# Kernel optimization log

Hardware: AMD Instinct MI355X
Metric: run time of the kernel (lower is better)

## Reference

```python
import jax, jax.numpy as jnp
import numpy as np

EPS = 1e-5
NUM_GROUPS = 16


def _deform_conv(x, offset, mask, weight):
    """Modulated deformable conv v2, 3x3, stride 1, pad 1, no bias.
    x: [B,C,H,W], offset: [B,18,H,W] (y,x interleaved per kernel point),
    mask: [B,9,H,W], weight: [O,C,3,3].
    """
    B, C, H, W = x.shape
    O = weight.shape[0]
    K = 9
    off = offset.reshape(B, K, 2, H, W)
    dy, dx = off[:, :, 0], off[:, :, 1]  # [B,K,H,W]
    # base sampling grid: output pixel + kernel tap offset (pad=1 -> taps -1..1)
    ky, kx = jnp.meshgrid(jnp.arange(3), jnp.arange(3), indexing='ij')
    ky = (ky.reshape(K) - 1).astype(x.dtype)
    kx = (kx.reshape(K) - 1).astype(x.dtype)
    iy = jnp.arange(H, dtype=x.dtype)[:, None]
    ix = jnp.arange(W, dtype=x.dtype)[None, :]
    py = iy[None, None] + ky[None, :, None, None] + dy  # [B,K,H,W]
    px = ix[None, None] + kx[None, :, None, None] + dx

    y0 = jnp.floor(py)
    x0 = jnp.floor(px)
    wy = py - y0  # grad flows to offsets via these weights
    wx = px - x0

    xf = x.reshape(B, C, H * W)

    def gather(yc, xc, w):
        # yc,xc,w: [B,K,H,W] float; returns weighted samples [B,C,K,H,W]
        valid = (yc >= 0) & (yc <= H - 1) & (xc >= 0) & (xc <= W - 1)
        yi = jnp.clip(yc, 0, H - 1).astype(jnp.int32)
        xi = jnp.clip(xc, 0, W - 1).astype(jnp.int32)
        idx = (yi * W + xi).reshape(B, K * H * W)
        g = jax.vmap(lambda xb, ib: xb[:, ib])(xf, idx)  # [B,C,K*H*W]
        g = g.reshape(B, C, K, H, W)
        wv = (w * valid.astype(x.dtype))[:, None]  # [B,1,K,H,W]
        return g * wv

    val = gather(y0, x0, (1 - wy) * (1 - wx))
    val = val + gather(y0, x0 + 1, (1 - wy) * wx)
    val = val + gather(y0 + 1, x0, wy * (1 - wx))
    val = val + gather(y0 + 1, x0 + 1, wy * wx)

    val = val * mask[:, None]  # modulation: [B,C,K,H,W] * [B,1,K,H,W]
    w = weight.reshape(O, C, K)
    return jnp.einsum('bckhw,ock->bohw', val, w)


def _group_norm(y, gamma, beta):
    B, O, H, W = y.shape
    g = y.reshape(B, NUM_GROUPS, O // NUM_GROUPS, H, W)
    mean = g.mean(axis=(2, 3, 4), keepdims=True)
    var = ((g - mean) ** 2).mean(axis=(2, 3, 4), keepdims=True)
    g = (g - mean) * jax.lax.rsqrt(var + EPS)
    y = g.reshape(B, O, H, W)
    return y * gamma[None, :, None, None] + beta[None, :, None, None]


def setup_inputs() -> dict:
    key = jax.random.key(0)
    k1, k2, k3, k4 = jax.random.split(key, 4)
    B, C, O, H, W = 8, 256, 256, 64, 64
    x = jax.random.normal(k1, (B, C, H, W), jnp.float32)
    offset = jax.random.normal(k2, (B, 18, H, W), jnp.float32)
    mask = jax.random.uniform(k3, (B, 9, H, W), jnp.float32)
    weight = jax.random.normal(k4, (O, C, 3, 3), jnp.float32) * 0.02
    gamma = jnp.ones((O,), jnp.float32)
    beta = jnp.zeros((O,), jnp.float32)
    return {"x": x, "offset": offset, "mask": mask, "weight": weight,
            "gamma": gamma, "beta": beta}


def reference(x, offset, mask, weight, gamma, beta):
    y = _deform_conv(x, offset, mask, weight)
    return _group_norm(y, gamma, beta)
```

## Files before the change

kernel.cpp:

```cpp
#include <hip/hip_runtime.h>
#include <hip/hip_fp16.h>
#include <math.h>

#define BB 8
#define CC 256
#define OO 256
#define HH 64
#define WW 64
#define KK 9
#define HWSZ 4096
#define CKSZ 2304
#define NG 16
#define OPG 16
#define EPSV 1e-5f

typedef _Float16 f16;
typedef f16 f16x8 __attribute__((ext_vector_type(8)));
typedef float f32x4 __attribute__((ext_vector_type(4)));

#define XH_ELEMS ((size_t)BB*HWSZ*CC)
#define WF_ELEMS ((size_t)OO*CKSZ)
#define CV_ELEMS ((size_t)BB*OO*HWSZ)
#define PSUM_FLOATS ((size_t)512*32)

__global__ __launch_bounds__(256) void x_transpose_k(
    const float* __restrict__ x, __half* __restrict__ xh)
{
  int blk = blockIdx.x;
  int b = blk >> 8; int rem = blk & 255;
  int c0 = (rem >> 6) * 64; int hw0 = (rem & 63) * 64;
  __shared__ float st[64][65];
  int t = threadIdx.x;
  #pragma unroll
  for (int i = 0; i < 16; ++i) {
    int idx = t + i*256; int c = idx >> 6, w = idx & 63;
    st[c][w] = x[((size_t)(b*CC + c0 + c))*HWSZ + hw0 + w];
  }
  __syncthreads();
  #pragma unroll
  for (int i = 0; i < 8; ++i) {
    int idx = t + i*256; int r = idx >> 5, cp = idx & 31;
    __half2 v = __floats2half2_rn(st[cp*2][r], st[cp*2+1][r]);
    *(__half2*)&xh[((size_t)(b*HWSZ) + hw0 + r)*CC + c0 + cp*2] = v;
  }
}

__global__ __launch_bounds__(256) void w_frag_k(
    const float* __restrict__ w, __half* __restrict__ wf)
{
  int i = blockIdx.x*256 + threadIdx.x;
  int e = i & 7, lane = (i >> 3) & 63, mi = (i >> 9) & 3;
  int ks = (i >> 11) & 1, wid = (i >> 12) & 3, cc = i >> 14;
  int k = cc >> 2, c0i = cc & 3;
  int o = wid*64 + mi*16 + (lane & 15);
  int c = c0i*64 + ks*32 + (lane >> 4)*8 + e;
  wf[i] = __float2half(w[(o*CC + c)*KK + k]);
}

template<int F16OUT>
__global__ __launch_bounds__(256, 3) void dcn_mfma_k(
    const float* __restrict__ off, const float* __restrict__ msk,
    const __half* __restrict__ xh, const __half* __restrict__ wf,
    float* __restrict__ out32, __half* __restrict__ conv16,
    float* __restrict__ psum)
{
  __shared__ __half sVl[2][64*64];
  __shared__ uint   sTapP[KK][64][4];
  __shared__ float  sRed[4][4][2];

  const int t = threadIdx.x;
  const int b = blockIdx.x & 7;
  const int h = blockIdx.x >> 3;

  const int lane = t & 63, wid = t >> 6;
  const int lr = lane & 15, lh = lane >> 4;
  const int gp = t >> 2, gq = t & 3;

  for (int s = t; s < KK*64; s += 256) {
    int k = s >> 6, p = s & 63;
    float dy = off[(((b*18) + 2*k    )*HH + h)*WW + p];
    float dx = off[(((b*18) + 2*k + 1)*HH + h)*WW + p];
    float m  = msk[(((b*KK) + k)*HH + h)*WW + p];
    float py = (float)(h + (k/3) - 1) + dy;
    float px = (float)(p + (k%3) - 1) + dx;
    float y0f = floorf(py), x0f = floorf(px);
    float wy = py - y0f, wx = px - x0f;
    int y0 = (int)y0f, x0 = (int)x0f;
    #pragma unroll
    for (int tap = 0; tap < 4; ++tap) {
      int yy = y0 + (tap >> 1), xx = x0 + (tap & 1);
      bool v = (yy >= 0) & (yy < HH) & (xx >= 0) & (xx < WW);
      float bw = ((tap >> 1) ? wy : 1.f - wy) * ((tap & 1) ? wx : 1.f - wx);
      float wgt = v ? bw * m : 0.f;
      int cy = min(max(yy, 0), HH-1), cx = min(max(xx, 0), WW-1);
      uint idx = (uint)(cy*WW + cx);
      sTapP[k][p][tap] = (idx << 16)
                       | (uint)__half_as_ushort(__float2half(wgt));
    }
  }
  __syncthreads();

  f32x4 acc[4][4];
  #pragma unroll
  for (int mi = 0; mi < 4; ++mi)
    #pragma unroll
    for (int ni = 0; ni < 4; ++ni) acc[mi][ni] = (f32x4){0.f,0.f,0.f,0.f};

  const char* xbase = (const char*)xh + (size_t)b * (HWSZ*CC*2);

  uint toff[4]; __half2 twv[4];
  #pragma unroll
  for (int i = 0; i < 4; ++i) {
    uint tp = sTapP[0][gp][i];
    toff[i] = (tp >> 16) << 9;
    twv[i]  = __half2half2(__ushort_as_half((unsigned short)(tp & 0xFFFFu)));
  }
  int tk = 0;

  auto combine_write = [&](uint4 r0, uint4 r1, uint4 r2, uint4 r3,
                           int oct, __half* dst) {
    const __half2* t0 = (const __half2*)&r0; const __half2* t1 = (const __half2*)&r1;
    const __half2* t2 = (const __half2*)&r2; const __half2* t3 = (const __half2*)&r3;
    __half2 o_[4];
    #pragma unroll
    for (int r = 0; r < 4; ++r)
      o_[r] = __hfma2(twv[0], t0[r], __hfma2(twv[1], t1[r],
              __hfma2(twv[2], t2[r], __hmul2(twv[3], t3[r]))));
    *(uint4*)&dst[gp*64 + ((oct ^ (gp & 7)) << 3)] = *(uint4*)o_;
  };

  {
    const char* cb = xbase + gq*16;
    uint4 a0 = *(const uint4*)(cb + toff[0]);
    uint4 a1 = *(const uint4*)(cb + toff[1]);
    uint4 a2 = *(const uint4*)(cb + toff[2]);
    uint4 a3 = *(const uint4*)(cb + toff[3]);
    uint4 b0 = *(const uint4*)(cb + toff[0] + 64);
    uint4 b1 = *(const uint4*)(cb + toff[1] + 64);
    uint4 b2 = *(const uint4*)(cb + toff[2] + 64);
    uint4 b3 = *(const uint4*)(cb + toff[3] + 64);
    combine_write(a0, a1, a2, a3, gq,     sVl[0]);
    combine_write(b0, b1, b2, b3, gq + 4, sVl[0]);
  }

  int cur = 0;
  for (int cc = 0; cc < 36; ++cc) {
    __syncthreads();

    const __half* wfp = wf + (size_t)(cc*4 + wid)*4096 + lane*8;
    f16x8 areg[2][4];
    #pragma unroll
    for (int ks = 0; ks < 2; ++ks)
      #pragma unroll
      for (int mi = 0; mi < 4; ++mi)
        areg[ks][mi] = *(const f16x8*)(wfp + (ks*4 + mi)*512);

    bool pf = (cc + 1 < 36);
    int kn = (cc+1) >> 2, c0n = ((cc+1) & 3) << 6;
    uint4 ga0, ga1, ga2, ga3, gb0, gb1, gb2, gb3;
    if (pf) {
      if (kn != tk) {
        #pragma unroll
        for (int i = 0; i < 4; ++i) {
          uint tp = sTapP[kn][gp][i];
          toff[i] = (tp >> 16) << 9;
          twv[i]  = __half2half2(__ushort_as_half((unsigned short)(tp & 0xFFFFu)));
        }
        tk = kn;
      }
      const char* cb = xbase + (size_t)(c0n*2) + gq*16;
      ga0 = *(const uint4*)(cb + toff[0]);
      ga1 = *(const uint4*)(cb + toff[1]);
      ga2 = *(const uint4*)(cb + toff[2]);
      ga3 = *(const uint4*)(cb + toff[3]);
      gb0 = *(const uint4*)(cb + toff[0] + 64);
      gb1 = *(const uint4*)(cb + toff[1] + 64);
      gb2 = *(const uint4*)(cb + toff[2] + 64);
      gb3 = *(const uint4*)(cb + toff[3] + 64);
    }

    #pragma unroll
    for (int ks = 0; ks < 2; ++ks) {
      f16x8 brg[4];
      #pragma unroll
      for (int ni = 0; ni < 4; ++ni) {
        int r = ni*16 + lr;
        brg[ni] = *(const f16x8*)&sVl[cur][r*64 + (((ks*4 + lh) ^ (r & 7)) << 3)];
      }
      #pragma unroll
      for (int mi = 0; mi < 4; ++mi)
        #pragma unroll
        for (int ni = 0; ni < 4; ++ni)
          acc[mi][ni] = __builtin_amdgcn_mfma_f32_16x16x32_f16(
              areg[ks][mi], brg[ni], acc[mi][ni], 0, 0, 0);
    }

    if (pf) {
      combine_write(ga0, ga1, ga2, ga3, gq,     sVl[cur ^ 1]);
      combine_write(gb0, gb1, gb2, gb3, gq + 4, sVl[cur ^ 1]);
      cur ^= 1;
    }
  }

  #pragma unroll
  for (int mi = 0; mi < 4; ++mi) {
    #pragma unroll
    for (int ni = 0; ni < 4; ++ni) {
      int ob = wid*64 + mi*16 + lh*4;
      int pp = ni*16 + lr;
      #pragma unroll
      for (int j = 0; j < 4; ++j) {
        size_t idx = ((size_t)(b*OO + ob + j))*HWSZ + h*WW + pp;
        if (F16OUT) conv16[idx] = __float2half(acc[mi][ni][j]);
        else        out32[idx] = acc[mi][ni][j];
      }
    }
  }

  if (F16OUT) {
    #pragma unroll
    for (int mi = 0; mi < 4; ++mi) {
      float s1 = 0.f, s2 = 0.f;
      #pragma unroll
      for (int ni = 0; ni < 4; ++ni)
        #pragma unroll
        for (int j = 0; j < 4; ++j) {
          float v = acc[mi][ni][j];
          s1 += v; s2 += v*v;
        }
      #pragma unroll
      for (int d = 32; d > 0; d >>= 1) {
        s1 += __shfl_xor(s1, d);
        s2 += __shfl_xor(s2, d);
      }
      if (lane == 0) { sRed[wid][mi][0] = s1; sRed[wid][mi][1] = s2; }
    }
    __syncthreads();
    if (t < 16) {
      psum[(size_t)blockIdx.x*32 + t*2]     = sRed[t >> 2][t & 3][0];
      psum[(size_t)blockIdx.x*32 + t*2 + 1] = sRed[t >> 2][t & 3][1];
    }
  }
}

__global__ __launch_bounds__(256) void gn_norm2_k(
    const __half* __restrict__ conv16, const float* __restrict__ psum,
    const float* __restrict__ gamma, const float* __restrict__ beta,
    float* __restrict__ out)
{
  int bid = blockIdx.x;
  int bo = bid >> 1;
  int b = bo >> 8, o = bo & 255;
  int g = o >> 4;
  float s1 = 0.f, s2 = 0.f;
  for (int hbl = 0; hbl < 64; ++hbl) {
    s1 += psum[(size_t)(hbl*8 + b)*32 + g*2];
    s2 += psum[(size_t)(hbl*8 + b)*32 + g*2 + 1];
  }
  const float invN = 1.f / (float)(OPG*HWSZ);
  float mean = s1 * invN;
  float var  = s2 * invN - mean*mean;
  float inv = rsqrtf(var + EPSV);
  float sc = gamma[o]*inv;
  float sh = beta[o] - mean*sc;

  size_t e0 = ((size_t)(b*OO + o))*HWSZ + (size_t)(bid & 1)*2048
            + (size_t)threadIdx.x*8;
  uint4 u = *(const uint4*)(conv16 + e0);
  const __half2* hh = (const __half2*)&u;
  float r[8];
  #pragma unroll
  for (int j = 0; j < 4; ++j) {
    float2 f = __half22float2(hh[j]);
    r[2*j] = f.x; r[2*j+1] = f.y;
  }
  *(float4*)&out[e0]     = make_float4(r[0]*sc+sh, r[1]*sc+sh, r[2]*sc+sh, r[3]*sc+sh);
  *(float4*)&out[e0 + 4] = make_float4(r[4]*sc+sh, r[5]*sc+sh, r[6]*sc+sh, r[7]*sc+sh);
}

__global__ __launch_bounds__(1024) void gn_stats_k(
    const float* __restrict__ out, float* __restrict__ stats)
{
  int bg = blockIdx.x;
  const float4* p = (const float4*)(out + (size_t)bg*OPG*HWSZ);
  const int n4 = OPG*HWSZ/4;
  float s1 = 0.f, s2 = 0.f;
  for (int i = threadIdx.x; i < n4; i += 1024) {
    float4 v = p[i];
    s1 += v.x + v.y + v.z + v.w;
    s2 += v.x*v.x + v.y*v.y + v.z*v.z + v.w*v.w;
  }
  #pragma unroll
  for (int o2 = 32; o2 > 0; o2 >>= 1) {
    s1 += __shfl_down(s1, o2);
    s2 += __shfl_down(s2, o2);
  }
  __shared__ float r1[16], r2[16];
  int wd = threadIdx.x >> 6, lane = threadIdx.x & 63;
  if (lane == 0) { r1[wd] = s1; r2[wd] = s2; }
  __syncthreads();
  if (threadIdx.x == 0) {
    float t1 = 0.f, t2 = 0.f;
    #pragma unroll
    for (int i = 0; i < 16; i++) { t1 += r1[i]; t2 += r2[i]; }
    const float invN = 1.f / (float)(OPG*HWSZ);
    float mean = t1 * invN;
    float var  = t2 * invN - mean*mean;
    stats[bg*2]   = mean;
    stats[bg*2+1] = var;
  }
}

__global__ __launch_bounds__(256) void gn_norm_k(
    float* __restrict__ out, const float* __restrict__ stats,
    const float* __restrict__ gamma, const float* __restrict__ beta)
{
  size_t i = (size_t)blockIdx.x*256 + threadIdx.x;
  const size_t n4 = (size_t)BB*OO*HWSZ/4;
  if (i >= n4) return;
  size_t base = i*4;
  int bo = (int)(base / HWSZ);
  int b = bo / OO, o = bo - b*OO;
  int g = o >> 4;
  float mean = stats[(b*NG+g)*2], var = stats[(b*NG+g)*2+1];
  float inv = rsqrtf(var + EPSV);
  float sc = gamma[o]*inv;
  float sh = beta[o] - mean*sc;
  float4 v = *(float4*)&out[base];
  v.x = v.x*sc + sh; v.y = v.y*sc + sh;
  v.z = v.z*sc + sh; v.w = v.w*sc + sh;
  *(float4*)&out[base] = v;
}

extern "C" void kernel_launch(void* const* d_in, const int* in_sizes, int n_in,
                              void* d_out, int out_size, void* d_ws, size_t ws_size,
                              hipStream_t stream) {
  const float* x      = (const float*)d_in[0];
  const float* offset = (const float*)d_in[1];
  const float* mask   = (const float*)d_in[2];
  const float* weight = (const float*)d_in[3];
  const float* gamma  = (const float*)d_in[4];
  const float* beta   = (const float*)d_in[5];
  float* out = (float*)d_out;

  __half* xh   = (__half*)d_ws;
  __half* wf   = xh + XH_ELEMS;
  __half* cv   = wf + WF_ELEMS;
  float* psum  = (float*)(cv + CV_ELEMS);

  const size_t need = (XH_ELEMS + WF_ELEMS + CV_ELEMS)*2 + PSUM_FLOATS*4 + 1024;

  x_transpose_k<<<BB*4*64, 256, 0, stream>>>(x, xh);
  w_frag_k<<<(int)(WF_ELEMS/256), 256, 0, stream>>>(weight, wf);

  if (ws_size >= need) {
    dcn_mfma_k<1><<<512, 256, 0, stream>>>(offset, mask, xh, wf,
                                           (float*)nullptr, cv, psum);
    gn_norm2_k<<<4096, 256, 0, stream>>>(cv, psum, gamma, beta, out);
  } else {
    float* stats = (float*)(wf + WF_ELEMS);
    dcn_mfma_k<0><<<512, 256, 0, stream>>>(offset, mask, xh, wf,
                                           out, (__half*)nullptr, (float*)nullptr);
    gn_stats_k<<<BB*NG, 1024, 0, stream>>>(out, stats);
    gn_norm_k<<<(int)((size_t)BB*OO*HWSZ/4 + 255)/256, 256, 0, stream>>>(
        out, stats, gamma, beta);
  }
}
```

Before: 89.66 us.

## Process two output rows per block with 8 waves sharing weight loads

```diff
diff --git a/kernel.cpp b/kernel.cpp
--- a/kernel.cpp
+++ b/kernel.cpp
@@ -21,7 +21,7 @@
 #define XH_ELEMS ((size_t)BB*HWSZ*CC)
 #define WF_ELEMS ((size_t)OO*CKSZ)
 #define CV_ELEMS ((size_t)BB*OO*HWSZ)
-#define PSUM_FLOATS ((size_t)512*32)
+#define NSTRIP 32
 
 __global__ __launch_bounds__(256) void x_transpose_k(
     const float* __restrict__ x, __half* __restrict__ xh)
@@ -50,39 +50,42 @@
 {
   int i = blockIdx.x*256 + threadIdx.x;
   int e = i & 7, lane = (i >> 3) & 63, mi = (i >> 9) & 3;
-  int ks = (i >> 11) & 1, wid = (i >> 12) & 3, cc = i >> 14;
+  int ks = (i >> 11) & 1, wm = (i >> 12) & 3, cc = i >> 14;
   int k = cc >> 2, c0i = cc & 3;
-  int o = wid*64 + mi*16 + (lane & 15);
+  int o = wm*64 + mi*16 + (lane & 15);
   int c = c0i*64 + ks*32 + (lane >> 4)*8 + e;
   wf[i] = __float2half(w[(o*CC + c)*KK + k]);
 }
 
 template<int F16OUT>
-__global__ __launch_bounds__(256, 3) void dcn_mfma_k(
+__global__ __launch_bounds__(512, 2) void dcn_mfma_k(
     const float* __restrict__ off, const float* __restrict__ msk,
     const __half* __restrict__ xh, const __half* __restrict__ wf,
     float* __restrict__ out32, __half* __restrict__ conv16,
     float* __restrict__ psum)
 {
-  __shared__ __half sVl[2][64*64];
-  __shared__ uint   sTapP[KK][64][4];
-  __shared__ float  sRed[4][4][2];
+  __shared__ __half sVl[2][128*64];
+  __shared__ uint   sTapP[KK][128][4];
+  __shared__ float  sRed[4][4][2][2];
 
   const int t = threadIdx.x;
   const int b = blockIdx.x & 7;
-  const int h = blockIdx.x >> 3;
+  const int strip = blockIdx.x >> 3;
+  const int h0 = strip * 2;
 
   const int lane = t & 63, wid = t >> 6;
+  const int wm = wid & 3, wn = wid >> 2;
   const int lr = lane & 15, lh = lane >> 4;
   const int gp = t >> 2, gq = t & 3;
 
-  for (int s = t; s < KK*64; s += 256) {
-    int k = s >> 6, p = s & 63;
-    float dy = off[(((b*18) + 2*k    )*HH + h)*WW + p];
-    float dx = off[(((b*18) + 2*k + 1)*HH + h)*WW + p];
-    float m  = msk[(((b*KK) + k)*HH + h)*WW + p];
+  for (int s = t; s < KK*128; s += 512) {
+    int k = s >> 7, p = s & 127;
+    int h = h0 + (p >> 6), w = p & 63;
+    float dy = off[(((b*18) + 2*k    )*HH + h)*WW + w];
+    float dx = off[(((b*18) + 2*k + 1)*HH + h)*WW + w];
+    float m  = msk[(((b*KK) + k)*HH + h)*WW + w];
     float py = (float)(h + (k/3) - 1) + dy;
-    float px = (float)(p + (k%3) - 1) + dx;
+    float px = (float)(w + (k%3) - 1) + dx;
     float y0f = floorf(py), x0f = floorf(px);
     float wy = py - y0f, wx = px - x0f;
     int y0 = (int)y0f, x0 = (int)x0f;
@@ -147,7 +150,7 @@
   for (int cc = 0; cc < 36; ++cc) {
     __syncthreads();
 
-    const __half* wfp = wf + (size_t)(cc*4 + wid)*4096 + lane*8;
+    const __half* wfp = wf + (size_t)(cc*4 + wm)*4096 + lane*8;
     f16x8 areg[2][4];
     #pragma unroll
     for (int ks = 0; ks < 2; ++ks)
@@ -184,7 +187,7 @@
       f16x8 brg[4];
       #pragma unroll
       for (int ni = 0; ni < 4; ++ni) {
-        int r = ni*16 + lr;
+        int r = wn*64 + ni*16 + lr;
         brg[ni] = *(const f16x8*)&sVl[cur][r*64 + (((ks*4 + lh) ^ (r & 7)) << 3)];
       }
       #pragma unroll
@@ -206,11 +209,11 @@
   for (int mi = 0; mi < 4; ++mi) {
     #pragma unroll
     for (int ni = 0; ni < 4; ++ni) {
-      int ob = wid*64 + mi*16 + lh*4;
-      int pp = ni*16 + lr;
+      int ob = wm*64 + mi*16 + lh*4;
+      int pp = wn*64 + ni*16 + lr;
       #pragma unroll
       for (int j = 0; j < 4; ++j) {
-        size_t idx = ((size_t)(b*OO + ob + j))*HWSZ + h*WW + pp;
+        size_t idx = ((size_t)(b*OO + ob + j))*HWSZ + strip*128 + pp;
         if (F16OUT) conv16[idx] = __float2half(acc[mi][ni][j]);
         else        out32[idx] = acc[mi][ni][j];
       }
@@ -233,12 +236,14 @@
         s1 += __shfl_xor(s1, d);
         s2 += __shfl_xor(s2, d);
       }
-      if (lane == 0) { sRed[wid][mi][0] = s1; sRed[wid][mi][1] = s2; }
+      if (lane == 0) { sRed[wm][mi][wn][0] = s1; sRed[wm][mi][wn][1] = s2; }
     }
     __syncthreads();
     if (t < 16) {
-      psum[(size_t)blockIdx.x*32 + t*2]     = sRed[t >> 2][t & 3][0];
-      psum[(size_t)blockIdx.x*32 + t*2 + 1] = sRed[t >> 2][t & 3][1];
+      float s1 = sRed[t >> 2][t & 3][0][0] + sRed[t >> 2][t & 3][1][0];
+      float s2 = sRed[t >> 2][t & 3][0][1] + sRed[t >> 2][t & 3][1][1];
+      psum[(size_t)blockIdx.x*32 + t*2]     = s1;
+      psum[(size_t)blockIdx.x*32 + t*2 + 1] = s2;
     }
   }
 }
@@ -253,9 +258,9 @@
   int b = bo >> 8, o = bo & 255;
   int g = o >> 4;
   float s1 = 0.f, s2 = 0.f;
-  for (int hbl = 0; hbl < 64; ++hbl) {
-    s1 += psum[(size_t)(hbl*8 + b)*32 + g*2];
-    s2 += psum[(size_t)(hbl*8 + b)*32 + g*2 + 1];
+  for (int st = 0; st < NSTRIP; ++st) {
+    s1 += psum[(size_t)(st*8 + b)*32 + g*2];
+    s2 += psum[(size_t)(st*8 + b)*32 + g*2 + 1];
   }
   const float invN = 1.f / (float)(OPG*HWSZ);
   float mean = s1 * invN;
@@ -348,19 +353,21 @@
   __half* cv   = wf + WF_ELEMS;
   float* psum  = (float*)(cv + CV_ELEMS);
 
-  const size_t need = (XH_ELEMS + WF_ELEMS + CV_ELEMS)*2 + PSUM_FLOATS*4 + 1024;
+  const size_t need = (XH_ELEMS + WF_ELEMS + CV_ELEMS)*2
+                    + (size_t)BB*NSTRIP*32*4 + 1024;
 
   x_transpose_k<<<BB*4*64, 256, 0, stream>>>(x, xh);
   w_frag_k<<<(int)(WF_ELEMS/256), 256, 0, stream>>>(weight, wf);
 
   if (ws_size >= need) {
-    dcn_mfma_k<1><<<512, 256, 0, stream>>>(offset, mask, xh, wf,
-                                           (float*)nullptr, cv, psum);
+    dcn_mfma_k<1><<<BB*NSTRIP, 512, 0, stream>>>(offset, mask, xh, wf,
+                                                 (float*)nullptr, cv, psum);
     gn_norm2_k<<<4096, 256, 0, stream>>>(cv, psum, gamma, beta, out);
   } else {
     float* stats = (float*)(wf + WF_ELEMS);
-    dcn_mfma_k<0><<<512, 256, 0, stream>>>(offset, mask, xh, wf,
-                                           out, (__half*)nullptr, (float*)nullptr);
+    dcn_mfma_k<0><<<BB*NSTRIP, 512, 0, stream>>>(offset, mask, xh, wf,
+                                                 out, (__half*)nullptr,
+                                                 (float*)nullptr);
     gn_stats_k<<<BB*NG, 1024, 0, stream>>>(out, stats);
     gn_norm_k<<<(int)((size_t)BB*OO*HWSZ/4 + 255)/256, 256, 0, stream>>>(
         out, stats, gamma, beta);
```

Result: faster. 87.55 us (-2.4%).
